# Performance work log

Measured on AMD Instinct MI355X. Metric: run time of the kernel, lower is better.

The kernel has to match this reference:

```python
import jax, jax.numpy as jnp
import numpy as np

B, D, H, K = 32768, 256, 8192, 32  # tokens, d_in, hidden latents, topk
EPS = float(np.finfo(np.float32).eps)


def setup_inputs() -> dict:
    key = jax.random.key(0)
    k0, k1, k2 = jax.random.split(key, 3)
    x = jax.random.normal(k0, (B, D), jnp.float32)
    W_enc = jax.random.normal(k1, (H, D), jnp.float32) * 0.02
    b_enc = jnp.zeros((H,), jnp.float32)
    # decoder initialized as encoder clone with unit-norm rows (set_decoder_norm_to_unit_norm)
    W_dec0 = jax.random.normal(k2, (H, D), jnp.float32) * 0.02
    W_dec = W_dec0 / (jnp.linalg.norm(W_dec0, axis=1, keepdims=True) + EPS)
    b_dec = jnp.zeros((D,), jnp.float32)
    return {"x": x, "W_enc": W_enc, "b_enc": b_enc, "W_dec": W_dec, "b_dec": b_dec}


def reference(x, W_enc, b_enc, W_dec, b_dec):
    # sae_in = x - b_dec; pre_acts = relu(encoder(sae_in))
    sae_in = x - b_dec
    pre_acts = jax.nn.relu(sae_in @ W_enc.T + b_enc)  # [B, H]
    # topk_activation: keep top-K values per row, zeros elsewhere; then z @ W_dec.
    # Equivalent (same math, no dense scatter): gather the K active decoder rows
    # and take the weighted sum.
    vals, idx = jax.lax.top_k(pre_acts, K)              # [B, K]
    x_reconstructed = jnp.einsum('bk,bkd->bd', vals, W_dec[idx]) + b_dec  # [B, D]
    return x_reconstructed
```

## Files before the change

kernel.cpp:

```cpp
#include <hip/hip_runtime.h>

#define B_TOK 32768
#define D_IN  256
#define H_LAT 8192
#define TOPK  32
#define MT    64
#define NT    128
#define NCH   (H_LAT / NT)
#define CAP   144
#define DELTA 0.016f

typedef __attribute__((ext_vector_type(4))) float f32x4;
typedef __attribute__((ext_vector_type(8))) short bf16x8;

__device__ __forceinline__ unsigned short f2bf(float f) {
    unsigned u = __float_as_uint(f);
    return (unsigned short)((u + 0x7fffu + ((u >> 16) & 1u)) >> 16);
}
__device__ __forceinline__ float bf2f(unsigned short u) {
    return __uint_as_float((unsigned)u << 16);
}

__global__ __launch_bounds__(256)
void conv_kernel(const float* __restrict__ W, unsigned short* __restrict__ Wbf,
                 float* __restrict__ s2w, const float* __restrict__ Wd,
                 unsigned short* __restrict__ Wdbf) {
    const int total4 = (H_LAT * D_IN) / 4;
    float acc = 0.0f;
    for (int j = blockIdx.x * blockDim.x + threadIdx.x; j < total4;
         j += gridDim.x * blockDim.x) {
        const int e4   = j & 1;
        const int lane = (j >> 1) & 63;
        const int c8   = (j >> 7) & 7;
        const int ct16 = j >> 10;
        const int h = ct16 * 16 + (lane & 15);
        const int k = c8 * 32 + (lane >> 4) * 8 + e4 * 4;
        const float4 v = *(const float4*)(W + (size_t)h * D_IN + k);
        acc += v.x * v.x + v.y * v.y + v.z * v.z + v.w * v.w;
        ushort4 o;
        o.x = f2bf(v.x); o.y = f2bf(v.y); o.z = f2bf(v.z); o.w = f2bf(v.w);
        ((ushort4*)Wbf)[j] = o;
    }
    for (int i = blockIdx.x * blockDim.x + threadIdx.x; i < total4;
         i += gridDim.x * blockDim.x) {
        const float4 v = ((const float4*)Wd)[i];
        ushort4 o;
        o.x = f2bf(v.x); o.y = f2bf(v.y); o.z = f2bf(v.z); o.w = f2bf(v.w);
        ((ushort4*)Wdbf)[i] = o;
    }
#pragma unroll
    for (int off = 32; off > 0; off >>= 1) acc += __shfl_down(acc, off, 64);
    if ((threadIdx.x & 63) == 0) atomicAdd(s2w, acc);
}

__global__ __launch_bounds__(512, 4)
void sae_main(const float* __restrict__ x, const float* __restrict__ W_enc,
              const float* __restrict__ b_enc, const float* __restrict__ W_dec,
              const float* __restrict__ b_dec, float* __restrict__ out,
              const unsigned short* __restrict__ Wbf, const float* __restrict__ s2w,
              const unsigned short* __restrict__ Wdbf) {
    __shared__ __align__(16) char smem[32768 + MT * CAP * 4];
    __shared__ int   cnt[MT];
    __shared__ float thr[MT];

    unsigned short* A = (unsigned short*)smem;
    auto pool = reinterpret_cast<unsigned (*)[CAP]>(smem + 32768);
    unsigned short* ext_i = (unsigned short*)smem;
    float*          ext_v = (float*)(smem + MT * 64 * 2);

    const int tid  = threadIdx.x;
    const int row0 = blockIdx.x * MT;
    const int wave = tid >> 6, lane = tid & 63;
    const int l15 = lane & 15, quad = lane >> 4;

    if (tid < MT) { cnt[tid] = 0; thr[tid] = 0.0f; }
    __syncthreads();

    {
        const int r = tid >> 3, q = tid & 7;
        const float* xr = x + (size_t)(row0 + r) * D_IN + q * 32;
        const float* bd = b_dec + q * 32;
        unsigned short* dst = A + ((r >> 4) * 8 + q) * 512 + (r & 15) * 8;
        float s2 = 0.0f;
#pragma unroll
        for (int j = 0; j < 4; ++j) {
            const float4 a = ((const float4*)xr)[2 * j];
            const float4 b = ((const float4*)xr)[2 * j + 1];
            const float4 da = ((const float4*)bd)[2 * j];
            const float4 db = ((const float4*)bd)[2 * j + 1];
            float v[8] = {a.x - da.x, a.y - da.y, a.z - da.z, a.w - da.w,
                          b.x - db.x, b.y - db.y, b.z - db.z, b.w - db.w};
            ushort4 p0, p1;
            p0.x = f2bf(v[0]); p0.y = f2bf(v[1]); p0.z = f2bf(v[2]); p0.w = f2bf(v[3]);
            p1.x = f2bf(v[4]); p1.y = f2bf(v[5]); p1.z = f2bf(v[6]); p1.w = f2bf(v[7]);
#pragma unroll
            for (int e = 0; e < 8; ++e) s2 += v[e] * v[e];
            *(ushort4*)(dst + j * 128)     = p0;
            *(ushort4*)(dst + j * 128 + 4) = p1;
        }
        atomicAdd(&thr[r], s2);
    }
    __syncthreads();
    if (tid < MT) {
        const float s2wm = s2w[0] * (1.0f / ((float)H_LAT * (float)D_IN));
        thr[tid] = 2.3f * sqrtf(s2wm * thr[tid]);
    }
    __syncthreads();

    float thrv[4][4];
#pragma unroll
    for (int mt = 0; mt < 4; ++mt)
#pragma unroll
        for (int qi = 0; qi < 4; ++qi) thrv[mt][qi] = thr[mt * 16 + quad * 4 + qi];

    const unsigned short* bp = Wbf + (size_t)(wave * 8) * 512 + lane * 8;
    const unsigned short* ap = A + lane * 8;
    const float* bep = b_enc + wave * 16 + l15;
    int col0 = wave * 16 + l15;

    int pos[4][4];
    auto collect = [&](const f32x4 (&ac)[4], int cbase) {
        const unsigned colk = (unsigned)(8191 - cbase);
#pragma unroll
        for (int mt = 0; mt < 4; ++mt)
#pragma unroll
            for (int qi = 0; qi < 4; ++qi) {
                pos[mt][qi] = -1;
                if (ac[mt][qi] > thrv[mt][qi])
                    pos[mt][qi] = atomicAdd(&cnt[mt * 16 + quad * 4 + qi], 1);
            }
#pragma unroll
        for (int mt = 0; mt < 4; ++mt)
#pragma unroll
            for (int qi = 0; qi < 4; ++qi) {
                if ((unsigned)pos[mt][qi] < CAP)
                    pool[mt * 16 + quad * 4 + qi][pos[mt][qi]] =
                        ((unsigned)f2bf(ac[mt][qi]) << 13) | colk;
            }
    };

    for (int g = 0; g < NCH; g += 2) {
        const float bv0 = bep[0], bv1 = bep[NT];

        f32x4 acc0[4], acc1[4];
#pragma unroll
        for (int mt = 0; mt < 4; ++mt) {
            acc0[mt] = {bv0, bv0, bv0, bv0};
            acc1[mt] = {bv1, bv1, bv1, bv1};
        }

#pragma unroll
        for (int c8 = 0; c8 < 8; ++c8) {
            const bf16x8 a0 = *(const bf16x8*)(ap + (0 * 8 + c8) * 512);
            const bf16x8 a1 = *(const bf16x8*)(ap + (1 * 8 + c8) * 512);
            const bf16x8 a2 = *(const bf16x8*)(ap + (2 * 8 + c8) * 512);
            const bf16x8 a3 = *(const bf16x8*)(ap + (3 * 8 + c8) * 512);
            const bf16x8 w0 = *(const bf16x8*)(bp + c8 * 512);
            const bf16x8 w1 = *(const bf16x8*)(bp + 32768 + c8 * 512);
            acc0[0] = __builtin_amdgcn_mfma_f32_16x16x32_bf16(a0, w0, acc0[0], 0, 0, 0);
            acc0[1] = __builtin_amdgcn_mfma_f32_16x16x32_bf16(a1, w0, acc0[1], 0, 0, 0);
            acc0[2] = __builtin_amdgcn_mfma_f32_16x16x32_bf16(a2, w0, acc0[2], 0, 0, 0);
            acc0[3] = __builtin_amdgcn_mfma_f32_16x16x32_bf16(a3, w0, acc0[3], 0, 0, 0);
            acc1[0] = __builtin_amdgcn_mfma_f32_16x16x32_bf16(a0, w1, acc1[0], 0, 0, 0);
            acc1[1] = __builtin_amdgcn_mfma_f32_16x16x32_bf16(a1, w1, acc1[1], 0, 0, 0);
            acc1[2] = __builtin_amdgcn_mfma_f32_16x16x32_bf16(a2, w1, acc1[2], 0, 0, 0);
            acc1[3] = __builtin_amdgcn_mfma_f32_16x16x32_bf16(a3, w1, acc1[3], 0, 0, 0);
        }

        collect(acc0, col0);
        collect(acc1, col0 + NT);

        bp  += 2 * 32768;
        bep += 2 * NT;
        col0 += 2 * NT;
    }
    __syncthreads();

    {
        const int rbase = wave * 8;
        for (int rr = 0; rr < 8; ++rr) {
            const int r = rbase + rr;
            const int n = min(cnt[r], CAP);
            unsigned p[3]; int rk[3];
            const int S = (n <= 128) ? 2 : 3;
#pragma unroll
            for (int e = 0; e < 3; ++e) {
                const int c = e * 64 + lane;
                p[e] = (c < n) ? pool[r][c] : (unsigned)(c + 1);
                rk[e] = 0;
            }
            if (S == 2) {
                for (int s = 0; s < 64; ++s) {
                    const int src = (lane + s) & 63;
                    const unsigned q0 = (unsigned)__shfl((int)p[0], src, 64);
                    const unsigned q1 = (unsigned)__shfl((int)p[1], src, 64);
                    rk[0] += (q0 > p[0]) + (q1 > p[0]);
                    rk[1] += (q0 > p[1]) + (q1 > p[1]);
                }
            } else {
                for (int s = 0; s < 64; ++s) {
                    const int src = (lane + s) & 63;
#pragma unroll
                    for (int e = 0; e < 3; ++e) {
                        const unsigned q = (unsigned)__shfl((int)p[e], src, 64);
#pragma unroll
                        for (int a = 0; a < 3; ++a) rk[a] += (q > p[a]);
                    }
                }
            }
#pragma unroll
            for (int e = 0; e < 3; ++e) {
                if (e < S && rk[e] < 64) {
                    if (p[e] >= 8192u) {
                        ext_i[r * 64 + rk[e]] = (unsigned short)(8191 - (p[e] & 0x1fffu));
                        ext_v[r * 64 + rk[e]] = __uint_as_float((p[e] >> 13) << 16);
                    } else {
                        ext_i[r * 64 + rk[e]] = (unsigned short)(0x2000 + rk[e]);
                        ext_v[r * 64 + rk[e]] = 0.0f;
                    }
                }
            }
        }
    }
    __syncthreads();

    {
        const int r = tid & 63, c = tid >> 6;
        const float v32 = ext_v[r * 64 + TOPK - 1];
        __syncthreads();
        const float* xr = x + (size_t)(row0 + r) * D_IN;
        for (int j = c; j < 64; j += 8) {
            const float va = ext_v[r * 64 + j];
            const int   h  = ext_i[r * 64 + j];
            if (h < H_LAT && fabsf(va - v32) <= DELTA) {
                const float* wr_ = W_enc + (size_t)h * D_IN;
                float s = 0.0f;
                for (int kk = 0; kk < D_IN / 4; ++kk) {
                    const float4 xv = ((const float4*)xr)[kk];
                    const float4 dv = ((const float4*)b_dec)[kk];
                    const float4 wv = ((const float4*)wr_)[kk];
                    s = fmaf(xv.x - dv.x, wv.x, s);
                    s = fmaf(xv.y - dv.y, wv.y, s);
                    s = fmaf(xv.z - dv.z, wv.z, s);
                    s = fmaf(xv.w - dv.w, wv.w, s);
                }
                ext_v[r * 64 + j] = fmaxf(s + b_enc[h], 0.0f);
            }
        }
    }
    __syncthreads();

    {
        const int rbase = wave * 8;
        const float4 bd4 = *(const float4*)&b_dec[lane * 4];
        for (int rr = 0; rr < 8; ++rr) {
            const int r = rbase + rr;
            const float v = ext_v[r * 64 + lane];
            const int   h = ext_i[r * 64 + lane];
            int rank = 0;
            for (int s = 0; s < 64; ++s) {
                const int src = (lane + s) & 63;
                const float wv = __shfl(v, src, 64);
                const int   wh = __shfl(h, src, 64);
                rank += (wv > v) || (wv == v && wh < h);
            }
            if (rank < TOPK) { ext_v[r * 64 + rank] = v; ext_i[r * 64 + rank] = (unsigned short)h; }
            float4 o = bd4;
#pragma unroll 8
            for (int k = 0; k < TOPK; ++k) {
                const float vv = ext_v[r * 64 + k];
                const int   hh = ext_i[r * 64 + k];
                if (hh < H_LAT) {
                    const ushort4 w = *(const ushort4*)&Wdbf[(size_t)hh * D_IN + lane * 4];
                    o.x = fmaf(vv, bf2f(w.x), o.x); o.y = fmaf(vv, bf2f(w.y), o.y);
                    o.z = fmaf(vv, bf2f(w.z), o.z); o.w = fmaf(vv, bf2f(w.w), o.w);
                }
            }
            *(float4*)&out[(size_t)(row0 + r) * D_IN + lane * 4] = o;
        }
    }
}

extern "C" void kernel_launch(void* const* d_in, const int* in_sizes, int n_in,
                              void* d_out, int out_size, void* d_ws, size_t ws_size,
                              hipStream_t stream) {
    const float* x     = (const float*)d_in[0];
    const float* W_enc = (const float*)d_in[1];
    const float* b_enc = (const float*)d_in[2];
    const float* W_dec = (const float*)d_in[3];
    const float* b_dec = (const float*)d_in[4];
    float* out = (float*)d_out;

    const size_t wel = (size_t)H_LAT * D_IN;
    float* s2w = (float*)d_ws;
    unsigned short* Wbf  = (unsigned short*)((char*)d_ws + 256);
    unsigned short* Wdbf = Wbf + wel;

    hipMemsetAsync(d_ws, 0, 256, stream);
    conv_kernel<<<dim3(1024), dim3(256), 0, stream>>>(W_enc, Wbf, s2w, W_dec, Wdbf);
    sae_main<<<dim3(B_TOK / MT), dim3(512), 0, stream>>>(x, W_enc, b_enc, W_dec, b_dec,
                                                         out, Wbf, s2w, Wdbf);
}
```

Baseline: 532.0 us.

## Split candidate selection and decode into separate kernel; unroll GEMM over four chunks

The main kernel now only runs the bf16 MFMA encoder GEMM and candidate collection, then writes each row's candidate pool and count to global workspace. A new second kernel, one wave per row, does the rank sort, fp32 re-scoring of borderline candidates, final top-k and gather decode. This frees the serial per-block selection tail from the GEMM kernel's occupancy limits and gives it more parallelism. The GEMM loop also processes four column chunks per iteration instead of two, which raises register pressure and adds a round trip for the pool through global memory.

After: 543.2 us. +2.1%, slower.

```diff
diff --git a/kernel.cpp b/kernel.cpp
--- a/kernel.cpp
+++ b/kernel.cpp
@@ -54,19 +54,16 @@
 }
 
 __global__ __launch_bounds__(512, 4)
-void sae_main(const float* __restrict__ x, const float* __restrict__ W_enc,
-              const float* __restrict__ b_enc, const float* __restrict__ W_dec,
-              const float* __restrict__ b_dec, float* __restrict__ out,
+void sae_main(const float* __restrict__ x, const float* __restrict__ b_enc,
+              const float* __restrict__ b_dec,
               const unsigned short* __restrict__ Wbf, const float* __restrict__ s2w,
-              const unsigned short* __restrict__ Wdbf) {
+              unsigned* __restrict__ pool_g, int* __restrict__ cnt_g) {
     __shared__ __align__(16) char smem[32768 + MT * CAP * 4];
     __shared__ int   cnt[MT];
     __shared__ float thr[MT];
 
     unsigned short* A = (unsigned short*)smem;
     auto pool = reinterpret_cast<unsigned (*)[CAP]>(smem + 32768);
-    unsigned short* ext_i = (unsigned short*)smem;
-    float*          ext_v = (float*)(smem + MT * 64 * 2);
 
     const int tid  = threadIdx.x;
     const int row0 = blockIdx.x * MT;
@@ -139,14 +136,17 @@
             }
     };
 
-    for (int g = 0; g < NCH; g += 2) {
-        const float bv0 = bep[0], bv1 = bep[NT];
-
-        f32x4 acc0[4], acc1[4];
+    for (int g = 0; g < NCH; g += 4) {
+        const float bv0 = bep[0],      bv1 = bep[NT];
+        const float bv2 = bep[2 * NT], bv3 = bep[3 * NT];
+
+        f32x4 acc0[4], acc1[4], acc2[4], acc3[4];
 #pragma unroll
         for (int mt = 0; mt < 4; ++mt) {
             acc0[mt] = {bv0, bv0, bv0, bv0};
             acc1[mt] = {bv1, bv1, bv1, bv1};
+            acc2[mt] = {bv2, bv2, bv2, bv2};
+            acc3[mt] = {bv3, bv3, bv3, bv3};
         }
 
 #pragma unroll
@@ -157,6 +157,8 @@
             const bf16x8 a3 = *(const bf16x8*)(ap + (3 * 8 + c8) * 512);
             const bf16x8 w0 = *(const bf16x8*)(bp + c8 * 512);
             const bf16x8 w1 = *(const bf16x8*)(bp + 32768 + c8 * 512);
+            const bf16x8 w2 = *(const bf16x8*)(bp + 65536 + c8 * 512);
+            const bf16x8 w3 = *(const bf16x8*)(bp + 98304 + c8 * 512);
             acc0[0] = __builtin_amdgcn_mfma_f32_16x16x32_bf16(a0, w0, acc0[0], 0, 0, 0);
             acc0[1] = __builtin_amdgcn_mfma_f32_16x16x32_bf16(a1, w0, acc0[1], 0, 0, 0);
             acc0[2] = __builtin_amdgcn_mfma_f32_16x16x32_bf16(a2, w0, acc0[2], 0, 0, 0);
@@ -165,120 +167,130 @@
             acc1[1] = __builtin_amdgcn_mfma_f32_16x16x32_bf16(a1, w1, acc1[1], 0, 0, 0);
             acc1[2] = __builtin_amdgcn_mfma_f32_16x16x32_bf16(a2, w1, acc1[2], 0, 0, 0);
             acc1[3] = __builtin_amdgcn_mfma_f32_16x16x32_bf16(a3, w1, acc1[3], 0, 0, 0);
+            acc2[0] = __builtin_amdgcn_mfma_f32_16x16x32_bf16(a0, w2, acc2[0], 0, 0, 0);
+            acc2[1] = __builtin_amdgcn_mfma_f32_16x16x32_bf16(a1, w2, acc2[1], 0, 0, 0);
+            acc2[2] = __builtin_amdgcn_mfma_f32_16x16x32_bf16(a2, w2, acc2[2], 0, 0, 0);
+            acc2[3] = __builtin_amdgcn_mfma_f32_16x16x32_bf16(a3, w2, acc2[3], 0, 0, 0);
+            acc3[0] = __builtin_amdgcn_mfma_f32_16x16x32_bf16(a0, w3, acc3[0], 0, 0, 0);
+            acc3[1] = __builtin_amdgcn_mfma_f32_16x16x32_bf16(a1, w3, acc3[1], 0, 0, 0);
+            acc3[2] = __builtin_amdgcn_mfma_f32_16x16x32_bf16(a2, w3, acc3[2], 0, 0, 0);
+            acc3[3] = __builtin_amdgcn_mfma_f32_16x16x32_bf16(a3, w3, acc3[3], 0, 0, 0);
         }
 
         collect(acc0, col0);
         collect(acc1, col0 + NT);
-
-        bp  += 2 * 32768;
-        bep += 2 * NT;
-        col0 += 2 * NT;
+        collect(acc2, col0 + 2 * NT);
+        collect(acc3, col0 + 3 * NT);
+
+        bp  += 4 * 32768;
+        bep += 4 * NT;
+        col0 += 4 * NT;
     }
     __syncthreads();
 
     {
-        const int rbase = wave * 8;
-        for (int rr = 0; rr < 8; ++rr) {
-            const int r = rbase + rr;
-            const int n = min(cnt[r], CAP);
-            unsigned p[3]; int rk[3];
-            const int S = (n <= 128) ? 2 : 3;
+        unsigned* pg = pool_g + (size_t)row0 * CAP;
+        const unsigned* ps = (const unsigned*)pool;
+        for (int i = tid; i < MT * CAP; i += 512) pg[i] = ps[i];
+        if (tid < MT) cnt_g[row0 + tid] = cnt[tid];
+    }
+}
+
+__global__ __launch_bounds__(512, 4)
+void sae_select(const float* __restrict__ x, const float* __restrict__ W_enc,
+                const float* __restrict__ b_enc, const float* __restrict__ b_dec,
+                float* __restrict__ out, const unsigned short* __restrict__ Wdbf,
+                const unsigned* __restrict__ pool_g, const int* __restrict__ cnt_g) {
+    __shared__ unsigned short ext_i[8][64];
+    __shared__ float          ext_v[8][64];
+
+    const int tid = threadIdx.x, wave = tid >> 6, lane = tid & 63;
+    const int r = blockIdx.x * 8 + wave;
+    const unsigned* pr = pool_g + (size_t)r * CAP;
+    const int n = min(cnt_g[r], CAP);
+
+    unsigned p[3]; int rk[3];
+    const int S = (n <= 128) ? 2 : 3;
+#pragma unroll
+    for (int e = 0; e < 3; ++e) {
+        const int c = e * 64 + lane;
+        p[e] = (c < n) ? pr[c] : (unsigned)(c + 1);
+        rk[e] = 0;
+    }
+    if (S == 2) {
+        for (int s = 0; s < 64; ++s) {
+            const int src = (lane + s) & 63;
+            const unsigned q0 = (unsigned)__shfl((int)p[0], src, 64);
+            const unsigned q1 = (unsigned)__shfl((int)p[1], src, 64);
+            rk[0] += (q0 > p[0]) + (q1 > p[0]);
+            rk[1] += (q0 > p[1]) + (q1 > p[1]);
+        }
+    } else {
+        for (int s = 0; s < 64; ++s) {
+            const int src = (lane + s) & 63;
 #pragma unroll
             for (int e = 0; e < 3; ++e) {
-                const int c = e * 64 + lane;
-                p[e] = (c < n) ? pool[r][c] : (unsigned)(c + 1);
-                rk[e] = 0;
+                const unsigned q = (unsigned)__shfl((int)p[e], src, 64);
+#pragma unroll
+                for (int a = 0; a < 3; ++a) rk[a] += (q > p[a]);
             }
-            if (S == 2) {
-                for (int s = 0; s < 64; ++s) {
-                    const int src = (lane + s) & 63;
-                    const unsigned q0 = (unsigned)__shfl((int)p[0], src, 64);
-                    const unsigned q1 = (unsigned)__shfl((int)p[1], src, 64);
-                    rk[0] += (q0 > p[0]) + (q1 > p[0]);
-                    rk[1] += (q0 > p[1]) + (q1 > p[1]);
-                }
+        }
+    }
+#pragma unroll
+    for (int e = 0; e < 3; ++e) {
+        if (e < S && rk[e] < 64) {
+            if (p[e] >= 8192u) {
+                ext_i[wave][rk[e]] = (unsigned short)(8191 - (p[e] & 0x1fffu));
+                ext_v[wave][rk[e]] = __uint_as_float((p[e] >> 13) << 16);
             } else {
-                for (int s = 0; s < 64; ++s) {
-                    const int src = (lane + s) & 63;
-#pragma unroll
-                    for (int e = 0; e < 3; ++e) {
-                        const unsigned q = (unsigned)__shfl((int)p[e], src, 64);
-#pragma unroll
-                        for (int a = 0; a < 3; ++a) rk[a] += (q > p[a]);
-                    }
-                }
+                ext_i[wave][rk[e]] = (unsigned short)(0x2000 + rk[e]);
+                ext_v[wave][rk[e]] = 0.0f;
             }
-#pragma unroll
-            for (int e = 0; e < 3; ++e) {
-                if (e < S && rk[e] < 64) {
-                    if (p[e] >= 8192u) {
-                        ext_i[r * 64 + rk[e]] = (unsigned short)(8191 - (p[e] & 0x1fffu));
-                        ext_v[r * 64 + rk[e]] = __uint_as_float((p[e] >> 13) << 16);
-                    } else {
-                        ext_i[r * 64 + rk[e]] = (unsigned short)(0x2000 + rk[e]);
-                        ext_v[r * 64 + rk[e]] = 0.0f;
-                    }
-                }
-            }
-        }
-    }
-    __syncthreads();
-
-    {
-        const int r = tid & 63, c = tid >> 6;
-        const float v32 = ext_v[r * 64 + TOPK - 1];
-        __syncthreads();
-        const float* xr = x + (size_t)(row0 + r) * D_IN;
-        for (int j = c; j < 64; j += 8) {
-            const float va = ext_v[r * 64 + j];
-            const int   h  = ext_i[r * 64 + j];
-            if (h < H_LAT && fabsf(va - v32) <= DELTA) {
-                const float* wr_ = W_enc + (size_t)h * D_IN;
-                float s = 0.0f;
-                for (int kk = 0; kk < D_IN / 4; ++kk) {
-                    const float4 xv = ((const float4*)xr)[kk];
-                    const float4 dv = ((const float4*)b_dec)[kk];
-                    const float4 wv = ((const float4*)wr_)[kk];
-                    s = fmaf(xv.x - dv.x, wv.x, s);
-                    s = fmaf(xv.y - dv.y, wv.y, s);
-                    s = fmaf(xv.z - dv.z, wv.z, s);
-                    s = fmaf(xv.w - dv.w, wv.w, s);
-                }
-                ext_v[r * 64 + j] = fmaxf(s + b_enc[h], 0.0f);
-            }
-        }
-    }
-    __syncthreads();
-
-    {
-        const int rbase = wave * 8;
-        const float4 bd4 = *(const float4*)&b_dec[lane * 4];
-        for (int rr = 0; rr < 8; ++rr) {
-            const int r = rbase + rr;
-            const float v = ext_v[r * 64 + lane];
-            const int   h = ext_i[r * 64 + lane];
-            int rank = 0;
-            for (int s = 0; s < 64; ++s) {
-                const int src = (lane + s) & 63;
-                const float wv = __shfl(v, src, 64);
-                const int   wh = __shfl(h, src, 64);
-                rank += (wv > v) || (wv == v && wh < h);
-            }
-            if (rank < TOPK) { ext_v[r * 64 + rank] = v; ext_i[r * 64 + rank] = (unsigned short)h; }
-            float4 o = bd4;
+        }
+    }
+
+    const float v32 = ext_v[wave][TOPK - 1];
+    const float va  = ext_v[wave][lane];
+    const int   h   = ext_i[wave][lane];
+    float v = va;
+    if (h < H_LAT && fabsf(va - v32) <= DELTA) {
+        const float* xr  = x + (size_t)r * D_IN;
+        const float* wr_ = W_enc + (size_t)h * D_IN;
+        float s = 0.0f;
+        for (int kk = 0; kk < D_IN / 4; ++kk) {
+            const float4 xv = ((const float4*)xr)[kk];
+            const float4 dv = ((const float4*)b_dec)[kk];
+            const float4 wv = ((const float4*)wr_)[kk];
+            s = fmaf(xv.x - dv.x, wv.x, s);
+            s = fmaf(xv.y - dv.y, wv.y, s);
+            s = fmaf(xv.z - dv.z, wv.z, s);
+            s = fmaf(xv.w - dv.w, wv.w, s);
+        }
+        v = fmaxf(s + b_enc[h], 0.0f);
+    }
+
+    int rank = 0;
+    for (int s = 0; s < 64; ++s) {
+        const int src = (lane + s) & 63;
+        const float wv = __shfl(v, src, 64);
+        const int   wh = __shfl(h, src, 64);
+        rank += (wv > v) || (wv == v && wh < h);
+    }
+    if (rank < TOPK) { ext_v[wave][rank] = v; ext_i[wave][rank] = (unsigned short)h; }
+
+    const float4 bd4 = *(const float4*)&b_dec[lane * 4];
+    float4 o = bd4;
 #pragma unroll 8
-            for (int k = 0; k < TOPK; ++k) {
-                const float vv = ext_v[r * 64 + k];
-                const int   hh = ext_i[r * 64 + k];
-                if (hh < H_LAT) {
-                    const ushort4 w = *(const ushort4*)&Wdbf[(size_t)hh * D_IN + lane * 4];
-                    o.x = fmaf(vv, bf2f(w.x), o.x); o.y = fmaf(vv, bf2f(w.y), o.y);
-                    o.z = fmaf(vv, bf2f(w.z), o.z); o.w = fmaf(vv, bf2f(w.w), o.w);
-                }
-            }
-            *(float4*)&out[(size_t)(row0 + r) * D_IN + lane * 4] = o;
-        }
-    }
+    for (int k = 0; k < TOPK; ++k) {
+        const float vv = ext_v[wave][k];
+        const int   hh = ext_i[wave][k];
+        if (hh < H_LAT) {
+            const ushort4 w = *(const ushort4*)&Wdbf[(size_t)hh * D_IN + lane * 4];
+            o.x = fmaf(vv, bf2f(w.x), o.x); o.y = fmaf(vv, bf2f(w.y), o.y);
+            o.z = fmaf(vv, bf2f(w.z), o.z); o.w = fmaf(vv, bf2f(w.w), o.w);
+        }
+    }
+    *(float4*)&out[(size_t)r * D_IN + lane * 4] = o;
 }
 
 extern "C" void kernel_launch(void* const* d_in, const int* in_sizes, int n_in,
@@ -295,9 +307,13 @@
     float* s2w = (float*)d_ws;
     unsigned short* Wbf  = (unsigned short*)((char*)d_ws + 256);
     unsigned short* Wdbf = Wbf + wel;
+    unsigned* pool_g = (unsigned*)(Wdbf + wel);
+    int* cnt_g = (int*)(pool_g + (size_t)B_TOK * CAP);
 
     hipMemsetAsync(d_ws, 0, 256, stream);
     conv_kernel<<<dim3(1024), dim3(256), 0, stream>>>(W_enc, Wbf, s2w, W_dec, Wdbf);
-    sae_main<<<dim3(B_TOK / MT), dim3(512), 0, stream>>>(x, W_enc, b_enc, W_dec, b_dec,
-                                                         out, Wbf, s2w, Wdbf);
-}
+    sae_main<<<dim3(B_TOK / MT), dim3(512), 0, stream>>>(x, b_enc, b_dec,
+                                                         Wbf, s2w, pool_g, cnt_g);
+    sae_select<<<dim3(B_TOK / 8), dim3(512), 0, stream>>>(x, W_enc, b_enc, b_dec,
+                                                          out, Wdbf, pool_g, cnt_g);
+}
```
